# Kernel tuning notes

Hardware: AMD Instinct MI355X
Metric: run time of the kernel (lower is better)

The kernel has to match this reference:

```python
import jax, jax.numpy as jnp
import numpy as np

B, H, L, E, MODES = 32, 8, 4096, 64, 64


def setup_inputs() -> dict:
    key = jax.random.key(0)
    kx, kw, ki = jax.random.split(key, 3)
    x = jax.random.normal(kx, (B, H, L, E), dtype=jnp.float32)
    # nn.Parameter(torch.randn(E, E, modes, 2) / sqrt(E))
    weights = jax.random.normal(kw, (E, E, MODES, 2), dtype=jnp.float32) / np.sqrt(E)
    # register_buffer: sorted random permutation of [0, seq_len//2) truncated to modes (unique)
    index = jnp.sort(jax.random.permutation(ki, L // 2)[:MODES]).astype(jnp.int64)
    return {"x": x, "weights": weights, "index": index}


def reference(x, weights, index):
    # x: [B, H, L, E]
    Bs, Hs, Ls, Es = x.shape
    xt = jnp.swapaxes(x, -1, -2)                 # [B, H, E, L]
    x_ft = jnp.fft.rfft(xt, axis=-1)             # [B, H, E, L//2+1] complex64
    w_c = weights[..., 0] + 1j * weights[..., 1]  # [E, E, modes] complex
    sel = x_ft[..., index]                       # gather selected modes: [B, H, E, modes]
    out_sel = jnp.einsum('bhei,eoi->bhoi', sel, w_c)  # [B, H, E_out, modes]
    out_ft = jnp.zeros_like(x_ft).at[..., index].set(out_sel)  # scatter into zero spectrum
    y = jnp.fft.irfft(out_ft, n=Ls, axis=-1)     # [B, H, E, L]
    return jnp.swapaxes(y, -1, -2)               # [B, H, L, E]
```

## Files before the change

kernel.cpp:

```cpp
#include <hip/hip_runtime.h>
#include <hip/hip_bf16.h>
#include <math.h>

#define LTOT   4096
#define EDIM   64
#define NMODES 64
#define BH     256
#define TWO_PI 6.28318530717958647692f

typedef float f32x4 __attribute__((ext_vector_type(4)));
typedef short s16x8 __attribute__((ext_vector_type(8)));

__device__ inline unsigned short f2bf(float f) {
    unsigned u = __builtin_bit_cast(unsigned, f);
    u += 0x7fff + ((u >> 16) & 1);
    return (unsigned short)(u >> 16);
}
__device__ inline unsigned packbf(float lo, float hi) {
    float2 t; t.x = lo; t.y = hi;
    __hip_bfloat162 h = __float22bfloat162_rn(t);
    unsigned r;
    __builtin_memcpy(&r, &h, 4);
    return r;
}
__device__ inline float bf2f(unsigned lo16) {
    return __builtin_bit_cast(float, lo16 << 16);
}

__global__ __launch_bounds__(256) void k_tables(const int* __restrict__ index,
                                                const float* __restrict__ w,
                                                unsigned short* __restrict__ Tm,
                                                unsigned short* __restrict__ Tt,
                                                unsigned* __restrict__ wt2) {
    int b = blockIdx.x, t = threadIdx.x;
    if (b < 256) {
        int k = b >> 2, f = index[k];
        int lq = b & 3;
        #pragma unroll
        for (int i = 0; i < 4; ++i) {
            int l = lq * 1024 + i * 256 + t;
            int m = (f * l) & (LTOT - 1);
            float th = (float)m * (TWO_PI / (float)LTOT);
            float s, c; sincosf(th, &s, &c);
            Tm[(size_t)(2 * k) * LTOT + l]     = f2bf(c);
            Tm[(size_t)(2 * k + 1) * LTOT + l] = f2bf(-s);
        }
    } else if (b < 256 + 1024) {
        int l = (b - 256) * 4 + (t >> 6);
        int k = t & 63, f = index[k];
        int m = (f * l) & (LTOT - 1);
        float th = (float)m * (TWO_PI / (float)LTOT);
        float s, c; sincosf(th, &s, &c);
        ((unsigned*)Tt)[l * 64 + k] = packbf(c, s);
    } else {
        int i = (b - 1280) * 256 + t;
        int e = i >> 12, o = (i >> 6) & 63, k = i & 63;
        float2 v = ((const float2*)w)[i];
        wt2[((size_t)(e * 64 + k)) * 64 + o] = packbf(v.x, v.y);
    }
}

__global__ __launch_bounds__(256, 5) void k_stage1(const float* __restrict__ x,
                                                   const unsigned short* __restrict__ Tm,
                                                   unsigned* __restrict__ XpB) {
    int bh = blockIdx.x >> 2, part = blockIdx.x & 3;
    const float* xb = x + ((size_t)bh * LTOT + part * 1024) * EDIM;
    __shared__ unsigned xT[64 * 68];

    int t = threadIdx.x;
    int q = t & 15, lp0 = t >> 4;
    int lane = t & 63, w = t >> 6;
    int r = lane & 15, kb8 = lane >> 4;
    int es = w & 1, ms = w >> 1;
    unsigned swzW = ((unsigned)(q & 7)) << 2;

    f32x4 acc[2][4];
    #pragma unroll
    for (int i = 0; i < 2; ++i)
        #pragma unroll
        for (int n = 0; n < 4; ++n) acc[i][n] = (f32x4)0.f;

    float4 xn[8];
    {
        #pragma unroll
        for (int p = 0; p < 4; ++p) {
            const float* bp = xb + (size_t)(2 * (lp0 + p * 16)) * EDIM + 4 * q;
            xn[2 * p]     = *(const float4*)bp;
            xn[2 * p + 1] = *(const float4*)(bp + EDIM);
        }
    }
    for (int t8 = 0; t8 < 8; ++t8) {
        #pragma unroll
        for (int p = 0; p < 4; ++p) {
            float A0[4] = {xn[2*p].x, xn[2*p].y, xn[2*p].z, xn[2*p].w};
            float A1[4] = {xn[2*p+1].x, xn[2*p+1].y, xn[2*p+1].z, xn[2*p+1].w};
            #pragma unroll
            for (int j = 0; j < 4; ++j)
                xT[(4 * q + j) * 68 + (((unsigned)(lp0 + p * 16)) ^ swzW)] = packbf(A0[j], A1[j]);
        }
        __syncthreads();
        if (t8 < 7) {
            const float* tb = xb + (size_t)((t8 + 1) * 128) * EDIM;
            #pragma unroll
            for (int p = 0; p < 4; ++p) {
                const float* bp = tb + (size_t)(2 * (lp0 + p * 16)) * EDIM + 4 * q;
                xn[2 * p]     = *(const float4*)bp;
                xn[2 * p + 1] = *(const float4*)(bp + EDIM);
            }
        }
        #pragma unroll
        for (int kk = 0; kk < 4; ++kk) {
            s16x8 af[2];
            #pragma unroll
            for (int sub = 0; sub < 2; ++sub) {
                int row = es * 32 + sub * 16 + r;
                unsigned swz = (((unsigned)sub) << 4) + (((unsigned)(r >> 2)) << 2);
                af[sub] = *(const s16x8*)(xT + row * 68 + (((unsigned)(kk * 16 + kb8 * 4)) ^ swz));
            }
            #pragma unroll
            for (int ns = 0; ns < 4; ++ns) {
                int m = ms * 64 + ns * 16 + r;
                s16x8 bf = *(const s16x8*)(Tm + (size_t)m * LTOT + part * 1024 + t8 * 128 + kk * 32 + kb8 * 8);
                acc[0][ns] = __builtin_amdgcn_mfma_f32_16x16x32_bf16(af[0], bf, acc[0][ns], 0, 0, 0);
                acc[1][ns] = __builtin_amdgcn_mfma_f32_16x16x32_bf16(af[1], bf, acc[1][ns], 0, 0, 0);
            }
        }
        __syncthreads();
    }

    unsigned* Xb = XpB + ((size_t)part * BH + bh) * (128 * 32);
    #pragma unroll
    for (int sub = 0; sub < 2; ++sub)
        #pragma unroll
        for (int ns = 0; ns < 4; ++ns) {
            int m   = ms * 64 + ns * 16 + r;
            int eu0 = es * 16 + sub * 8 + kb8 * 2;
            uint2 pv;
            pv.x = packbf(acc[sub][ns][0], acc[sub][ns][1]);
            pv.y = packbf(acc[sub][ns][2], acc[sub][ns][3]);
            *(uint2*)(Xb + m * 32 + eu0) = pv;
        }
}

__global__ __launch_bounds__(1024) void k_stage2(const unsigned* __restrict__ XpB,
                                                 const unsigned* __restrict__ wt2,
                                                 const int* __restrict__ index,
                                                 unsigned* __restrict__ ABo) {
    int bh = blockIdx.x;
    __shared__ float XsR[64 * 68];
    __shared__ float XsI[64 * 68];
    int t = threadIdx.x;

    #pragma unroll
    for (int i = 0; i < 4; ++i) {
        int idx = t + i * 1024;
        float lo = 0.f, hi = 0.f;
        #pragma unroll
        for (int p = 0; p < 4; ++p) {
            unsigned v = XpB[((size_t)p * BH + bh) * 4096 + idx];
            lo += bf2f(v & 0xffffu);
            hi += bf2f(v >> 16);
        }
        int m = idx >> 5, eu = idx & 31;
        float* plane = (m & 1) ? XsI : XsR;
        int k = m >> 1;
        plane[(2 * eu) * 68 + k]     = lo;
        plane[(2 * eu + 1) * 68 + k] = hi;
    }
    __syncthreads();

    int k = t & 63, og = t >> 6;
    int f = index[k];
    float cc = (f == 0 ? 1.0f : 2.0f) / (float)LTOT;
    int o0 = og * 4;
    float aR[4] = {}, aI[4] = {};
    #pragma unroll 4
    for (int e = 0; e < 64; ++e) {
        float xr = XsR[e * 68 + k];
        float xi = XsI[e * 68 + k];
        uint4 wv = *(const uint4*)&wt2[((size_t)(e * 64 + k)) * 64 + o0];
        unsigned wa[4] = {wv.x, wv.y, wv.z, wv.w};
        #pragma unroll
        for (int oi = 0; oi < 4; ++oi) {
            float wr = bf2f(wa[oi] & 0xffffu);
            float wi = bf2f(wa[oi] >> 16);
            aR[oi] += xr * wr - xi * wi;
            aI[oi] += xr * wi + xi * wr;
        }
    }
    #pragma unroll
    for (int oi = 0; oi < 4; ++oi) {
        float im = (f == 0) ? 0.0f : -cc * aI[oi];
        ABo[((size_t)bh * 64 + o0 + oi) * 64 + k] = packbf(cc * aR[oi], im);
    }
}

#define S3P16 136
__global__ __launch_bounds__(256, 4) void k_stage3(const unsigned short* __restrict__ Tt,
                                                   const unsigned* __restrict__ ABo,
                                                   float* __restrict__ y) {
    int bh = blockIdx.x >> 2, qtr = blockIdx.x & 3;
    __shared__ unsigned short ABl[64 * S3P16];
    int t = threadIdx.x;
    int lane = t & 63, wave = t >> 6;
    int r = lane & 15, kb8 = lane >> 4;

    {
        const unsigned* src = ABo + (size_t)bh * 4096;
        unsigned* dst = (unsigned*)ABl;
        #pragma unroll
        for (int i = 0; i < 16; ++i) {
            int idx = t + i * 256;
            int o = idx >> 6, c = idx & 63;
            dst[o * (S3P16 / 2) + c] = src[idx];
        }
    }
    __syncthreads();

    s16x8 afr[4][4];
    #pragma unroll
    for (int es = 0; es < 4; ++es)
        #pragma unroll
        for (int ks = 0; ks < 4; ++ks)
            afr[es][ks] = *(const s16x8*)(ABl + (es * 16 + r) * S3P16 + ks * 32 + kb8 * 8);

    for (int it = 0; it < 16; ++it) {
        int ltile = qtr * 1024 + it * 64 + wave * 16;
        s16x8 btf[4];
        #pragma unroll
        for (int ks = 0; ks < 4; ++ks)
            btf[ks] = *(const s16x8*)(Tt + (size_t)(ltile + r) * 128 + ks * 32 + kb8 * 8);
        f32x4 acc[4];
        #pragma unroll
        for (int es = 0; es < 4; ++es) acc[es] = (f32x4)0.f;
        #pragma unroll
        for (int ks = 0; ks < 4; ++ks)
            #pragma unroll
            for (int es = 0; es < 4; ++es)
                acc[es] = __builtin_amdgcn_mfma_f32_16x16x32_bf16(afr[es][ks], btf[ks], acc[es], 0, 0, 0);
        float* yb = y + ((size_t)bh * LTOT + ltile + r) * EDIM;
        #pragma unroll
        for (int es = 0; es < 4; ++es)
            *(f32x4*)(yb + es * 16 + kb8 * 4) = acc[es];
    }
}

extern "C" void kernel_launch(void* const* d_in, const int* in_sizes, int n_in,
                              void* d_out, int out_size, void* d_ws, size_t ws_size,
                              hipStream_t stream) {
    const float* x     = (const float*)d_in[0];
    const float* wgt   = (const float*)d_in[1];
    const int*   index = (const int*)d_in[2];
    float* y  = (float*)d_out;
    float* ws = (float*)d_ws;

    unsigned short* Tm  = (unsigned short*)ws;
    unsigned short* Tt  = (unsigned short*)(ws + 262144);
    unsigned*       wt2 = (unsigned*)(ws + 524288);
    unsigned*       XpB = (unsigned*)(ws + 786432);
    unsigned*       ABo = (unsigned*)(ws + 4980736);

    hipLaunchKernelGGL(k_tables, dim3(2304),   dim3(256),  0, stream, index, wgt, Tm, Tt, wt2);
    hipLaunchKernelGGL(k_stage1, dim3(BH * 4), dim3(256),  0, stream, x, Tm, XpB);
    hipLaunchKernelGGL(k_stage2, dim3(BH),     dim3(1024), 0, stream, XpB, wt2, index, ABo);
    hipLaunchKernelGGL(k_stage3, dim3(BH * 4), dim3(256),  0, stream, Tt, ABo, y);
}
```

Before: 243.8 us.

## Widen stage1 to 512 threads, store fp32 partials, prefetch stage3 tiles

Stage1 now runs 512 threads per block, with each wave owning one 16-row slice, and writes fp32 partial spectra in an e-major layout instead of packed bf16. Stage2 reads those partials with vector loads and sums them. The weight-table write is made contiguous by transposing on the read side. Stage3 double-buffers the twiddle-tile fragments from the next iteration to hide load latency. The aim is more parallelism and better latency hiding in stage1 and stage3, at the cost of twice the intermediate memory traffic from fp32 partials and more register pressure.

Measured after the change: 273.2 us. 12.1% more time.

```diff
diff --git a/kernel.cpp b/kernel.cpp
--- a/kernel.cpp
+++ b/kernel.cpp
@@ -54,15 +54,15 @@
         ((unsigned*)Tt)[l * 64 + k] = packbf(c, s);
     } else {
         int i = (b - 1280) * 256 + t;
-        int e = i >> 12, o = (i >> 6) & 63, k = i & 63;
-        float2 v = ((const float2*)w)[i];
-        wt2[((size_t)(e * 64 + k)) * 64 + o] = packbf(v.x, v.y);
-    }
-}
-
-__global__ __launch_bounds__(256, 5) void k_stage1(const float* __restrict__ x,
+        int e = i >> 12, k = (i >> 6) & 63, o = i & 63;
+        float2 v = ((const float2*)w)[((size_t)e * 64 + o) * 64 + k];
+        wt2[i] = packbf(v.x, v.y);
+    }
+}
+
+__global__ __launch_bounds__(512, 8) void k_stage1(const float* __restrict__ x,
                                                    const unsigned short* __restrict__ Tm,
-                                                   unsigned* __restrict__ XpB) {
+                                                   float* __restrict__ Xp) {
     int bh = blockIdx.x >> 2, part = blockIdx.x & 3;
     const float* xb = x + ((size_t)bh * LTOT + part * 1024) * EDIM;
     __shared__ unsigned xT[64 * 68];
@@ -71,78 +71,64 @@
     int q = t & 15, lp0 = t >> 4;
     int lane = t & 63, w = t >> 6;
     int r = lane & 15, kb8 = lane >> 4;
-    int es = w & 1, ms = w >> 1;
+    int es = w & 3, ms = w >> 2;
     unsigned swzW = ((unsigned)(q & 7)) << 2;
-
-    f32x4 acc[2][4];
-    #pragma unroll
-    for (int i = 0; i < 2; ++i)
-        #pragma unroll
-        for (int n = 0; n < 4; ++n) acc[i][n] = (f32x4)0.f;
-
-    float4 xn[8];
+    int arow = es * 16 + r;
+    unsigned swzR = (((unsigned)(arow >> 2)) & 7u) << 2;
+
+    f32x4 acc[4];
+    acc[0] = (f32x4)0.f; acc[1] = (f32x4)0.f; acc[2] = (f32x4)0.f; acc[3] = (f32x4)0.f;
+
+    float4 xn[4];
     {
-        #pragma unroll
-        for (int p = 0; p < 4; ++p) {
-            const float* bp = xb + (size_t)(2 * (lp0 + p * 16)) * EDIM + 4 * q;
-            xn[2 * p]     = *(const float4*)bp;
-            xn[2 * p + 1] = *(const float4*)(bp + EDIM);
-        }
+        const float* bp = xb + (size_t)(2 * lp0) * EDIM + 4 * q;
+        xn[0] = *(const float4*)bp;
+        xn[1] = *(const float4*)(bp + EDIM);
+        xn[2] = *(const float4*)(bp + 64 * EDIM);
+        xn[3] = *(const float4*)(bp + 65 * EDIM);
     }
     for (int t8 = 0; t8 < 8; ++t8) {
-        #pragma unroll
-        for (int p = 0; p < 4; ++p) {
-            float A0[4] = {xn[2*p].x, xn[2*p].y, xn[2*p].z, xn[2*p].w};
-            float A1[4] = {xn[2*p+1].x, xn[2*p+1].y, xn[2*p+1].z, xn[2*p+1].w};
-            #pragma unroll
-            for (int j = 0; j < 4; ++j)
-                xT[(4 * q + j) * 68 + (((unsigned)(lp0 + p * 16)) ^ swzW)] = packbf(A0[j], A1[j]);
+        {
+            float A0[4] = {xn[0].x, xn[0].y, xn[0].z, xn[0].w};
+            float A1[4] = {xn[1].x, xn[1].y, xn[1].z, xn[1].w};
+            float A2[4] = {xn[2].x, xn[2].y, xn[2].z, xn[2].w};
+            float A3[4] = {xn[3].x, xn[3].y, xn[3].z, xn[3].w};
+            #pragma unroll
+            for (int j = 0; j < 4; ++j) {
+                xT[(4 * q + j) * 68 + (((unsigned)lp0)        ^ swzW)] = packbf(A0[j], A1[j]);
+                xT[(4 * q + j) * 68 + (((unsigned)(lp0 + 32)) ^ swzW)] = packbf(A2[j], A3[j]);
+            }
         }
         __syncthreads();
         if (t8 < 7) {
-            const float* tb = xb + (size_t)((t8 + 1) * 128) * EDIM;
-            #pragma unroll
-            for (int p = 0; p < 4; ++p) {
-                const float* bp = tb + (size_t)(2 * (lp0 + p * 16)) * EDIM + 4 * q;
-                xn[2 * p]     = *(const float4*)bp;
-                xn[2 * p + 1] = *(const float4*)(bp + EDIM);
-            }
+            const float* tb = xb + (size_t)((t8 + 1) * 128 + 2 * lp0) * EDIM + 4 * q;
+            xn[0] = *(const float4*)tb;
+            xn[1] = *(const float4*)(tb + EDIM);
+            xn[2] = *(const float4*)(tb + 64 * EDIM);
+            xn[3] = *(const float4*)(tb + 65 * EDIM);
         }
         #pragma unroll
         for (int kk = 0; kk < 4; ++kk) {
-            s16x8 af[2];
-            #pragma unroll
-            for (int sub = 0; sub < 2; ++sub) {
-                int row = es * 32 + sub * 16 + r;
-                unsigned swz = (((unsigned)sub) << 4) + (((unsigned)(r >> 2)) << 2);
-                af[sub] = *(const s16x8*)(xT + row * 68 + (((unsigned)(kk * 16 + kb8 * 4)) ^ swz));
-            }
+            s16x8 af = *(const s16x8*)(xT + arow * 68 + (((unsigned)(kk * 16 + kb8 * 4)) ^ swzR));
             #pragma unroll
             for (int ns = 0; ns < 4; ++ns) {
                 int m = ms * 64 + ns * 16 + r;
                 s16x8 bf = *(const s16x8*)(Tm + (size_t)m * LTOT + part * 1024 + t8 * 128 + kk * 32 + kb8 * 8);
-                acc[0][ns] = __builtin_amdgcn_mfma_f32_16x16x32_bf16(af[0], bf, acc[0][ns], 0, 0, 0);
-                acc[1][ns] = __builtin_amdgcn_mfma_f32_16x16x32_bf16(af[1], bf, acc[1][ns], 0, 0, 0);
+                acc[ns] = __builtin_amdgcn_mfma_f32_16x16x32_bf16(af, bf, acc[ns], 0, 0, 0);
             }
         }
         __syncthreads();
     }
 
-    unsigned* Xb = XpB + ((size_t)part * BH + bh) * (128 * 32);
-    #pragma unroll
-    for (int sub = 0; sub < 2; ++sub)
-        #pragma unroll
-        for (int ns = 0; ns < 4; ++ns) {
-            int m   = ms * 64 + ns * 16 + r;
-            int eu0 = es * 16 + sub * 8 + kb8 * 2;
-            uint2 pv;
-            pv.x = packbf(acc[sub][ns][0], acc[sub][ns][1]);
-            pv.y = packbf(acc[sub][ns][2], acc[sub][ns][3]);
-            *(uint2*)(Xb + m * 32 + eu0) = pv;
-        }
-}
-
-__global__ __launch_bounds__(1024) void k_stage2(const unsigned* __restrict__ XpB,
+    float* Xb = Xp + ((size_t)part * BH + bh) * (64 * 128);
+    #pragma unroll
+    for (int ns = 0; ns < 4; ++ns)
+        #pragma unroll
+        for (int g = 0; g < 4; ++g)
+            Xb[(es * 16 + kb8 * 4 + g) * 128 + ms * 64 + ns * 16 + r] = acc[ns][g];
+}
+
+__global__ __launch_bounds__(1024) void k_stage2(const float* __restrict__ Xp,
                                                  const unsigned* __restrict__ wt2,
                                                  const int* __restrict__ index,
                                                  unsigned* __restrict__ ABo) {
@@ -152,20 +138,17 @@
     int t = threadIdx.x;
 
     #pragma unroll
-    for (int i = 0; i < 4; ++i) {
+    for (int i = 0; i < 2; ++i) {
         int idx = t + i * 1024;
-        float lo = 0.f, hi = 0.f;
-        #pragma unroll
-        for (int p = 0; p < 4; ++p) {
-            unsigned v = XpB[((size_t)p * BH + bh) * 4096 + idx];
-            lo += bf2f(v & 0xffffu);
-            hi += bf2f(v >> 16);
-        }
-        int m = idx >> 5, eu = idx & 31;
-        float* plane = (m & 1) ? XsI : XsR;
-        int k = m >> 1;
-        plane[(2 * eu) * 68 + k]     = lo;
-        plane[(2 * eu + 1) * 68 + k] = hi;
+        f32x4 v = (f32x4)0.f;
+        #pragma unroll
+        for (int p = 0; p < 4; ++p)
+            v += ((const f32x4*)(Xp + ((size_t)p * BH + bh) * 8192))[idx];
+        int e = idx >> 5, k0 = (idx & 31) * 2;
+        XsR[e * 68 + k0]     = v.x;
+        XsI[e * 68 + k0]     = v.y;
+        XsR[e * 68 + k0 + 1] = v.z;
+        XsI[e * 68 + k0 + 1] = v.w;
     }
     __syncthreads();
 
@@ -224,20 +207,31 @@
         for (int ks = 0; ks < 4; ++ks)
             afr[es][ks] = *(const s16x8*)(ABl + (es * 16 + r) * S3P16 + ks * 32 + kb8 * 8);
 
+    s16x8 btf[2][4];
+    {
+        int lt0 = qtr * 1024 + wave * 16;
+        #pragma unroll
+        for (int ks = 0; ks < 4; ++ks)
+            btf[0][ks] = *(const s16x8*)(Tt + (size_t)(lt0 + r) * 128 + ks * 32 + kb8 * 8);
+    }
+    #pragma unroll 2
     for (int it = 0; it < 16; ++it) {
+        int cur = it & 1;
+        if (it < 15) {
+            int lt2 = qtr * 1024 + (it + 1) * 64 + wave * 16;
+            #pragma unroll
+            for (int ks = 0; ks < 4; ++ks)
+                btf[cur ^ 1][ks] = *(const s16x8*)(Tt + (size_t)(lt2 + r) * 128 + ks * 32 + kb8 * 8);
+        }
+        f32x4 acc[4];
+        #pragma unroll
+        for (int es = 0; es < 4; ++es) acc[es] = (f32x4)0.f;
+        #pragma unroll
+        for (int ks = 0; ks < 4; ++ks)
+            #pragma unroll
+            for (int es = 0; es < 4; ++es)
+                acc[es] = __builtin_amdgcn_mfma_f32_16x16x32_bf16(afr[es][ks], btf[cur][ks], acc[es], 0, 0, 0);
         int ltile = qtr * 1024 + it * 64 + wave * 16;
-        s16x8 btf[4];
-        #pragma unroll
-        for (int ks = 0; ks < 4; ++ks)
-            btf[ks] = *(const s16x8*)(Tt + (size_t)(ltile + r) * 128 + ks * 32 + kb8 * 8);
-        f32x4 acc[4];
-        #pragma unroll
-        for (int es = 0; es < 4; ++es) acc[es] = (f32x4)0.f;
-        #pragma unroll
-        for (int ks = 0; ks < 4; ++ks)
-            #pragma unroll
-            for (int es = 0; es < 4; ++es)
-                acc[es] = __builtin_amdgcn_mfma_f32_16x16x32_bf16(afr[es][ks], btf[ks], acc[es], 0, 0, 0);
         float* yb = y + ((size_t)bh * LTOT + ltile + r) * EDIM;
         #pragma unroll
         for (int es = 0; es < 4; ++es)
@@ -257,11 +251,11 @@
     unsigned short* Tm  = (unsigned short*)ws;
     unsigned short* Tt  = (unsigned short*)(ws + 262144);
     unsigned*       wt2 = (unsigned*)(ws + 524288);
-    unsigned*       XpB = (unsigned*)(ws + 786432);
-    unsigned*       ABo = (unsigned*)(ws + 4980736);
+    float*          Xp  = ws + 786432;
+    unsigned*       ABo = (unsigned*)(ws + 9175040);
 
     hipLaunchKernelGGL(k_tables, dim3(2304),   dim3(256),  0, stream, index, wgt, Tm, Tt, wt2);
-    hipLaunchKernelGGL(k_stage1, dim3(BH * 4), dim3(256),  0, stream, x, Tm, XpB);
-    hipLaunchKernelGGL(k_stage2, dim3(BH),     dim3(1024), 0, stream, XpB, wt2, index, ABo);
+    hipLaunchKernelGGL(k_stage1, dim3(BH * 4), dim3(512),  0, stream, x, Tm, Xp);
+    hipLaunchKernelGGL(k_stage2, dim3(BH),     dim3(1024), 0, stream, Xp, wt2, index, ABo);
     hipLaunchKernelGGL(k_stage3, dim3(BH * 4), dim3(256),  0, stream, Tt, ABo, y);
 }
```
